# Performance work log

Hardware: AMD Instinct MI355X
Metric: run time of the kernel (lower is better)

## Reference

```python
import jax, jax.numpy as jnp
import numpy as np

B, L, C = 32, 4096, 64
PL, PC = 64, 16          # patch sizes along L and C
NP = 256                 # num_patches
OUT = 512                # output_dim
FS = 1000.0              # sampling frequency -> T = 1/FS


def setup_inputs() -> dict:
    key = jax.random.key(0)
    ks = jax.random.split(key, 7)
    d_in = PL * (PC * 2)
    return {
        "x": jax.random.normal(ks[0], (B, L, C), dtype=jnp.float32),
        "start_L": jax.random.randint(ks[1], (B, NP), 0, L - PL + 1, dtype=jnp.int32),
        "start_C": jax.random.randint(ks[2], (B, NP), 0, C - PC + 1, dtype=jnp.int32),
        "w1": jax.random.normal(ks[3], (OUT, d_in), dtype=jnp.float32) / np.sqrt(d_in),
        "b1": jax.random.normal(ks[4], (OUT,), dtype=jnp.float32) * 0.01,
        "w2": jax.random.normal(ks[5], (OUT, OUT), dtype=jnp.float32) / np.sqrt(OUT),
        "b2": jax.random.normal(ks[6], (OUT,), dtype=jnp.float32) * 0.01,
    }


def reference(x, start_L, start_C, w1, b1, w2, b2):
    T = 1.0 / FS
    t = jnp.arange(L, dtype=jnp.float32) * T                      # [L]

    # patch index grids (wrapping, as in the torch module)
    idx_L = (start_L[:, :, None] + jnp.arange(PL, dtype=jnp.int32)) % L   # [B,NP,PL]
    idx_C = (start_C[:, :, None] + jnp.arange(PC, dtype=jnp.int32)) % C   # [B,NP,PC]

    # double gather: patches[b,p,i,j] = x[b, idx_L[b,p,i], idx_C[b,p,j]]
    b_idx = jnp.arange(B, dtype=jnp.int32)[:, None, None, None]
    patches = x[b_idx, idx_L[:, :, :, None], idx_C[:, :, None, :]]        # [B,NP,PL,PC]

    # time embedding gathered with the same L indices, broadcast over PC
    t_patches = jnp.broadcast_to(t[idx_L][:, :, :, None], (B, NP, PL, PC))

    feats = jnp.concatenate([patches, t_patches], axis=-1)                # [B,NP,PL,2*PC]
    feats = feats.reshape(B, NP, PL * 2 * PC)

    h = jnp.einsum('bpd,od->bpo', feats, w1) + b1
    h = jax.nn.silu(h)
    out = jnp.einsum('bpo,qo->bpq', h, w2) + b2                           # [B,NP,OUT]
    return out
```

## Files before the change

kernel.cpp:

```cpp
#include <hip/hip_runtime.h>
#include <hip/hip_bf16.h>
#include <stdint.h>

#define LL   4096
#define CCH  64
#define DOUT 512
#define MM   8192
#define TT   0.001f

using bf16 = __hip_bfloat16;
typedef __attribute__((ext_vector_type(8))) short bf16x8;
typedef __attribute__((ext_vector_type(4))) float f32x4;

__device__ __forceinline__ uint2 pack4_bf16(float a, float b, float c, float d) {
    union { bf16 h[4]; uint2 u; } p;
    p.h[0] = __float2bfloat16(a);
    p.h[1] = __float2bfloat16(b);
    p.h[2] = __float2bfloat16(c);
    p.h[3] = __float2bfloat16(d);
    return p.u;
}

__global__ __launch_bounds__(256) void prep(
    const float* __restrict__ w1, const float* __restrict__ b1,
    const float* __restrict__ w2,
    bf16* __restrict__ w1g, bf16* __restrict__ w2g,
    float* __restrict__ A1, float* __restrict__ C1)
{
    const int blk = blockIdx.x;
    if (blk < 512) {
        int g   = blk * 256 + threadIdx.x;
        int kk0 = (g & 7) * 4;
        int col = (g >> 3) & 511;
        int ic  = g >> 12;
        int l   = ic * 2 + (kk0 >> 4);
        int j0  = kk0 & 15;
        float4 v = *(const float4*)(w1 + (size_t)col * 2048 + l * 32 + j0);
        *(uint2*)(w1g + ((size_t)(ic * 512 + col) * 32 + kk0)) =
            pack4_bf16(v.x, v.y, v.z, v.w);
    } else if (blk < 768) {
        int g   = (blk - 512) * 256 + threadIdx.x;
        int kk0 = (g & 7) * 4;
        int col = (g >> 3) & 511;
        int ic2 = g >> 12;
        float4 v = *(const float4*)(w2 + (size_t)col * 512 + ic2 * 32 + kk0);
        *(uint2*)(w2g + ((size_t)(ic2 * 512 + col) * 32 + kk0)) =
            pack4_bf16(v.x, v.y, v.z, v.w);
    } else {
        const int o = (blk - 768) * 4 + (threadIdx.x >> 6);
        const int l = threadIdx.x & 63;
        const float* wr = w1 + (size_t)o * 2048 + l * 32 + 16;
        float s0 = 0.f;
#pragma unroll
        for (int j = 0; j < 16; ++j) s0 += wr[j];
        float s1 = (float)l * s0;
#pragma unroll
        for (int off = 32; off > 0; off >>= 1) {
            s0 += __shfl_down(s0, off);
            s1 += __shfl_down(s1, off);
        }
        if (l == 0) {
            A1[o] = TT * s0;
            C1[o] = b1[o] + TT * s1;
        }
    }
}

__global__ __launch_bounds__(512, 2) void mega(
    const float* __restrict__ x, const int* __restrict__ sLg,
    const int* __restrict__ sCg, const bf16* __restrict__ w1g,
    const bf16* __restrict__ w2g, const float* __restrict__ A1,
    const float* __restrict__ C1, const float* __restrict__ b2,
    float* __restrict__ out)
{
    __shared__ __align__(16) bf16 Asm[32 * 1024];
    bf16* const Hs = Asm;

    const int t    = threadIdx.x;
    const int lane = t & 63;
    const int wave = t >> 6;
    const int fr   = lane & 15;
    const int fq   = lane >> 4;
    const int m0   = blockIdx.x * 32;
    const int b    = m0 >> 8;

    {
        const int gr  = t >> 4;
        const int gs  = t & 15;
        const int gsl = sLg[m0 + gr];
        const int gsc = sCg[m0 + gr];
        const float* gx = x + ((size_t)b * LL + gsl + (gs >> 2)) * CCH
                            + gsc + (gs & 3) * 4;
        float4 xv[16];
#pragma unroll
        for (int p = 0; p < 16; ++p)
            xv[p] = *(const float4*)(gx + (size_t)p * 4 * CCH);
#pragma unroll
        for (int p = 0; p < 16; ++p) {
            const int l = 4 * p + (gs >> 2);
            const int u = l * 2 + ((gs & 3) >> 1);
            const int idx = gr * 1024 + ((u ^ (gr & 7)) * 8) + (gs & 1) * 4;
            *(uint2*)(Asm + idx) = pack4_bf16(xv[p].x, xv[p].y, xv[p].z, xv[p].w);
        }
    }
    __syncthreads();

    const bf16* const w1base = w1g + (size_t)(wave * 64 + fr) * 32 + fq * 8;
    f32x4 acc[2][4] = {};
    {
        bf16x8 bnx[4];
#pragma unroll
        for (int j = 0; j < 4; ++j)
            bnx[j] = *(const bf16x8*)(w1base + j * 512);
#pragma unroll
        for (int it = 0; it < 32; ++it) {
            bf16x8 bcur[4];
#pragma unroll
            for (int j = 0; j < 4; ++j) bcur[j] = bnx[j];
            if (it < 31) {
                const bf16* p = w1base + (size_t)(it + 1) * 16384;
#pragma unroll
                for (int j = 0; j < 4; ++j)
                    bnx[j] = *(const bf16x8*)(p + j * 512);
            }
            bf16x8 af[2];
#pragma unroll
            for (int i = 0; i < 2; ++i) {
                const int row = i * 16 + fr;
                const int u   = it * 4 + fq;
                af[i] = *(const bf16x8*)&Asm[row * 1024 + ((u ^ (row & 7)) * 8)];
            }
#pragma unroll
            for (int i = 0; i < 2; ++i)
#pragma unroll
                for (int j = 0; j < 4; ++j)
                    acc[i][j] = __builtin_amdgcn_mfma_f32_16x16x32_bf16(
                        af[i], bcur[j], acc[i][j], 0, 0, 0);
        }
    }
    __syncthreads();

    {
        float slr[2][4];
#pragma unroll
        for (int i = 0; i < 2; ++i)
#pragma unroll
            for (int rr = 0; rr < 4; ++rr)
                slr[i][rr] = (float)sLg[m0 + i * 16 + fq * 4 + rr];
#pragma unroll
        for (int j = 0; j < 4; ++j) {
            const int col = wave * 64 + j * 16 + fr;
            const float av = A1[col];
            const float cv = C1[col];
            const int c8 = col >> 3, c7 = col & 7;
#pragma unroll
            for (int i = 0; i < 2; ++i)
#pragma unroll
                for (int rr = 0; rr < 4; ++rr) {
                    const int row = i * 16 + fq * 4 + rr;
                    float v = acc[i][j][rr] + slr[i][rr] * av + cv;
                    v = v / (1.0f + __expf(-v));
                    Hs[row * 512 + ((c8 ^ (row & 7)) * 8) + c7] = __float2bfloat16(v);
                }
        }
    }
    __syncthreads();

    const bf16* const w2base = w2g + (size_t)(wave * 64 + fr) * 32 + fq * 8;
    f32x4 acc2[2][4] = {};
    {
        bf16x8 bnx[4];
#pragma unroll
        for (int j = 0; j < 4; ++j)
            bnx[j] = *(const bf16x8*)(w2base + j * 512);
#pragma unroll
        for (int it2 = 0; it2 < 16; ++it2) {
            bf16x8 bcur[4];
#pragma unroll
            for (int j = 0; j < 4; ++j) bcur[j] = bnx[j];
            if (it2 < 15) {
                const bf16* p = w2base + (size_t)(it2 + 1) * 16384;
#pragma unroll
                for (int j = 0; j < 4; ++j)
                    bnx[j] = *(const bf16x8*)(p + j * 512);
            }
            bf16x8 af[2];
#pragma unroll
            for (int i = 0; i < 2; ++i) {
                const int row = i * 16 + fr;
                const int u2  = it2 * 4 + fq;
                af[i] = *(const bf16x8*)&Hs[row * 512 + ((u2 ^ (row & 7)) * 8)];
            }
#pragma unroll
            for (int i = 0; i < 2; ++i)
#pragma unroll
                for (int j = 0; j < 4; ++j)
                    acc2[i][j] = __builtin_amdgcn_mfma_f32_16x16x32_bf16(
                        af[i], bcur[j], acc2[i][j], 0, 0, 0);
        }
    }

#pragma unroll
    for (int j = 0; j < 4; ++j) {
        const int col = wave * 64 + j * 16 + fr;
        const float bv = b2[col];
#pragma unroll
        for (int i = 0; i < 2; ++i)
#pragma unroll
            for (int rr = 0; rr < 4; ++rr) {
                const int row = m0 + i * 16 + fq * 4 + rr;
                out[(size_t)row * 512 + col] = acc2[i][j][rr] + bv;
            }
    }
}

extern "C" void kernel_launch(void* const* d_in, const int* in_sizes, int n_in,
                              void* d_out, int out_size, void* d_ws, size_t ws_size,
                              hipStream_t stream)
{
    const float* x  = (const float*)d_in[0];
    const int*   sL = (const int*)  d_in[1];
    const int*   sC = (const int*)  d_in[2];
    const float* w1 = (const float*)d_in[3];
    const float* b1 = (const float*)d_in[4];
    const float* w2 = (const float*)d_in[5];
    const float* b2 = (const float*)d_in[6];
    float* out = (float*)d_out;

    char* ws = (char*)d_ws;
    bf16*  w1g = (bf16*)ws;
    bf16*  w2g = (bf16*)(ws + (1 << 20));
    float* A1  = (float*)(ws + (1 << 20) + (1 << 19));
    float* C1  = A1 + DOUT;

    prep<<<896, 256, 0, stream>>>(w1, b1, w2, w1g, w2g, A1, C1);
    mega<<<MM / 32, 512, 0, stream>>>(x, sL, sC, w1g, w2g, A1, C1, b2, out);
}
```

Measured before the change: 123.5 us.

## Deepen weight prefetch to four stages and double-buffer LDS A fragments

Both GEMM loops now keep four iterations of weight fragments in flight in registers instead of one, and load the next iteration's LDS A fragments before issuing the current MFMAs. The second-GEMM weight prefetch, the A1/C1/b2 loads and the start_L values (cached in LDS) are moved earlier so they overlap the first GEMM epilogue. The aim is to hide global load latency under the MFMAs. The cost is many more VGPRs (16 bf16x8 per buffer), which could cause spills or lower occupancy under launch_bounds(512,2).

```diff
diff --git a/kernel.cpp b/kernel.cpp
--- a/kernel.cpp
+++ b/kernel.cpp
@@ -74,6 +74,7 @@
     float* __restrict__ out)
 {
     __shared__ __align__(16) bf16 Asm[32 * 1024];
+    __shared__ float slf[32];
     bf16* const Hs = Asm;
 
     const int t    = threadIdx.x;
@@ -89,6 +90,7 @@
         const int gs  = t & 15;
         const int gsl = sLg[m0 + gr];
         const int gsc = sCg[m0 + gr];
+        if (gs == 0) slf[gr] = (float)gsl;
         const float* gx = x + ((size_t)b * LL + gsl + (gs >> 2)) * CCH
                             + gsc + (gs & 3) * 4;
         float4 xv[16];
@@ -108,27 +110,37 @@
     const bf16* const w1base = w1g + (size_t)(wave * 64 + fr) * 32 + fq * 8;
     f32x4 acc[2][4] = {};
     {
-        bf16x8 bnx[4];
-#pragma unroll
-        for (int j = 0; j < 4; ++j)
-            bnx[j] = *(const bf16x8*)(w1base + j * 512);
+        bf16x8 bnx[4][4];
+#pragma unroll
+        for (int d = 0; d < 4; ++d)
+#pragma unroll
+            for (int j = 0; j < 4; ++j)
+                bnx[d][j] = *(const bf16x8*)(w1base + (size_t)d * 16384 + j * 512);
+        bf16x8 af[2];
+#pragma unroll
+        for (int i = 0; i < 2; ++i) {
+            const int row = i * 16 + fr;
+            af[i] = *(const bf16x8*)&Asm[row * 1024 + ((fq ^ (row & 7)) * 8)];
+        }
 #pragma unroll
         for (int it = 0; it < 32; ++it) {
             bf16x8 bcur[4];
 #pragma unroll
-            for (int j = 0; j < 4; ++j) bcur[j] = bnx[j];
+            for (int j = 0; j < 4; ++j) bcur[j] = bnx[it & 3][j];
+            if (it < 28) {
+                const bf16* p = w1base + (size_t)(it + 4) * 16384;
+#pragma unroll
+                for (int j = 0; j < 4; ++j)
+                    bnx[it & 3][j] = *(const bf16x8*)(p + j * 512);
+            }
+            bf16x8 afn[2];
             if (it < 31) {
-                const bf16* p = w1base + (size_t)(it + 1) * 16384;
-#pragma unroll
-                for (int j = 0; j < 4; ++j)
-                    bnx[j] = *(const bf16x8*)(p + j * 512);
-            }
-            bf16x8 af[2];
-#pragma unroll
-            for (int i = 0; i < 2; ++i) {
-                const int row = i * 16 + fr;
-                const int u   = it * 4 + fq;
-                af[i] = *(const bf16x8*)&Asm[row * 1024 + ((u ^ (row & 7)) * 8)];
+#pragma unroll
+                for (int i = 0; i < 2; ++i) {
+                    const int row = i * 16 + fr;
+                    const int u   = (it + 1) * 4 + fq;
+                    afn[i] = *(const bf16x8*)&Asm[row * 1024 + ((u ^ (row & 7)) * 8)];
+                }
             }
 #pragma unroll
             for (int i = 0; i < 2; ++i)
@@ -136,22 +148,41 @@
                 for (int j = 0; j < 4; ++j)
                     acc[i][j] = __builtin_amdgcn_mfma_f32_16x16x32_bf16(
                         af[i], bcur[j], acc[i][j], 0, 0, 0);
+            if (it < 31) {
+#pragma unroll
+                for (int i = 0; i < 2; ++i) af[i] = afn[i];
+            }
         }
     }
     __syncthreads();
 
+    const bf16* const w2base = w2g + (size_t)(wave * 64 + fr) * 32 + fq * 8;
+    bf16x8 bnx2[4][4];
+#pragma unroll
+    for (int d = 0; d < 4; ++d)
+#pragma unroll
+        for (int j = 0; j < 4; ++j)
+            bnx2[d][j] = *(const bf16x8*)(w2base + (size_t)d * 16384 + j * 512);
+    float avv[4], cvv[4];
+#pragma unroll
+    for (int j = 0; j < 4; ++j) {
+        const int col = wave * 64 + j * 16 + fr;
+        avv[j] = A1[col];
+        cvv[j] = C1[col];
+    }
+
     {
         float slr[2][4];
 #pragma unroll
         for (int i = 0; i < 2; ++i)
 #pragma unroll
             for (int rr = 0; rr < 4; ++rr)
-                slr[i][rr] = (float)sLg[m0 + i * 16 + fq * 4 + rr];
+                slr[i][rr] = slf[i * 16 + fq * 4 + rr];
 #pragma unroll
         for (int j = 0; j < 4; ++j) {
             const int col = wave * 64 + j * 16 + fr;
-            const float av = A1[col];
-            const float cv = C1[col];
+            const float av = avv[j];
+            const float cv = cvv[j];
             const int c8 = col >> 3, c7 = col & 7;
 #pragma unroll
             for (int i = 0; i < 2; ++i)
@@ -166,44 +197,54 @@
     }
     __syncthreads();
 
-    const bf16* const w2base = w2g + (size_t)(wave * 64 + fr) * 32 + fq * 8;
     f32x4 acc2[2][4] = {};
-    {
-        bf16x8 bnx[4];
-#pragma unroll
-        for (int j = 0; j < 4; ++j)
-            bnx[j] = *(const bf16x8*)(w2base + j * 512);
+    float bvv[4];
+#pragma unroll
+    for (int j = 0; j < 4; ++j) bvv[j] = b2[wave * 64 + j * 16 + fr];
+    {
+        bf16x8 af2[2];
+#pragma unroll
+        for (int i = 0; i < 2; ++i) {
+            const int row = i * 16 + fr;
+            af2[i] = *(const bf16x8*)&Hs[row * 512 + ((fq ^ (row & 7)) * 8)];
+        }
 #pragma unroll
         for (int it2 = 0; it2 < 16; ++it2) {
             bf16x8 bcur[4];
 #pragma unroll
-            for (int j = 0; j < 4; ++j) bcur[j] = bnx[j];
+            for (int j = 0; j < 4; ++j) bcur[j] = bnx2[it2 & 3][j];
+            if (it2 < 12) {
+                const bf16* p = w2base + (size_t)(it2 + 4) * 16384;
+#pragma unroll
+                for (int j = 0; j < 4; ++j)
+                    bnx2[it2 & 3][j] = *(const bf16x8*)(p + j * 512);
+            }
+            bf16x8 afn[2];
             if (it2 < 15) {
-                const bf16* p = w2base + (size_t)(it2 + 1) * 16384;
-#pragma unroll
-                for (int j = 0; j < 4; ++j)
-                    bnx[j] = *(const bf16x8*)(p + j * 512);
-            }
-            bf16x8 af[2];
-#pragma unroll
-            for (int i = 0; i < 2; ++i) {
-                const int row = i * 16 + fr;
-                const int u2  = it2 * 4 + fq;
-                af[i] = *(const bf16x8*)&Hs[row * 512 + ((u2 ^ (row & 7)) * 8)];
+#pragma unroll
+                for (int i = 0; i < 2; ++i) {
+                    const int row = i * 16 + fr;
+                    const int u2  = (it2 + 1) * 4 + fq;
+                    afn[i] = *(const bf16x8*)&Hs[row * 512 + ((u2 ^ (row & 7)) * 8)];
+                }
             }
 #pragma unroll
             for (int i = 0; i < 2; ++i)
 #pragma unroll
                 for (int j = 0; j < 4; ++j)
                     acc2[i][j] = __builtin_amdgcn_mfma_f32_16x16x32_bf16(
-                        af[i], bcur[j], acc2[i][j], 0, 0, 0);
+                        af2[i], bcur[j], acc2[i][j], 0, 0, 0);
+            if (it2 < 15) {
+#pragma unroll
+                for (int i = 0; i < 2; ++i) af2[i] = afn[i];
+            }
         }
     }
 
 #pragma unroll
     for (int j = 0; j < 4; ++j) {
         const int col = wave * 64 + j * 16 + fr;
-        const float bv = b2[col];
+        const float bv = bvv[j];
 #pragma unroll
         for (int i = 0; i < 2; ++i)
 #pragma unroll
```

New measurement: 121.4 us. No clear change (-1.6%).

## Double block threads to 1024 and halve per-wave column tile

Applied to the files above, without the earlier changes.

Launches 16 waves per block, each owning 32 output columns instead of 64, with a wider gather mapping. It also hoists the second GEMM weight prefetch and the bias/affine loads ahead of the SiLU stage, and caches start_L in shared memory. The aim is more waves to hide memory latency and overlap of weight loads with the activation stage. The tighter launch bounds may restrict registers and cause spills, and each wave reuses the A fragments less.

```diff
diff --git a/kernel.cpp b/kernel.cpp
--- a/kernel.cpp
+++ b/kernel.cpp
@@ -66,7 +66,7 @@
     }
 }
 
-__global__ __launch_bounds__(512, 2) void mega(
+__global__ __launch_bounds__(1024, 4) void mega(
     const float* __restrict__ x, const int* __restrict__ sLg,
     const int* __restrict__ sCg, const bf16* __restrict__ w1g,
     const bf16* __restrict__ w2g, const float* __restrict__ A1,
@@ -74,6 +74,7 @@
     float* __restrict__ out)
 {
     __shared__ __align__(16) bf16 Asm[32 * 1024];
+    __shared__ float slf[32];
     bf16* const Hs = Asm;
 
     const int t    = threadIdx.x;
@@ -85,42 +86,45 @@
     const int b    = m0 >> 8;
 
     {
-        const int gr  = t >> 4;
-        const int gs  = t & 15;
+        const int gr  = t >> 5;
+        const int gs  = t & 31;
         const int gsl = sLg[m0 + gr];
         const int gsc = sCg[m0 + gr];
-        const float* gx = x + ((size_t)b * LL + gsl + (gs >> 2)) * CCH
-                            + gsc + (gs & 3) * 4;
-        float4 xv[16];
-#pragma unroll
-        for (int p = 0; p < 16; ++p)
-            xv[p] = *(const float4*)(gx + (size_t)p * 4 * CCH);
-#pragma unroll
-        for (int p = 0; p < 16; ++p) {
-            const int l = 4 * p + (gs >> 2);
-            const int u = l * 2 + ((gs & 3) >> 1);
-            const int idx = gr * 1024 + ((u ^ (gr & 7)) * 8) + (gs & 1) * 4;
+        if (gs == 0) slf[gr] = (float)gsl;
+        const int c4 = gs & 3;
+        const int l0 = gs >> 2;
+        const float* gx = x + ((size_t)b * LL + gsl + l0) * CCH
+                            + gsc + c4 * 4;
+        float4 xv[8];
+#pragma unroll
+        for (int p = 0; p < 8; ++p)
+            xv[p] = *(const float4*)(gx + (size_t)p * 8 * CCH);
+#pragma unroll
+        for (int p = 0; p < 8; ++p) {
+            const int l = p * 8 + l0;
+            const int u = l * 2 + (c4 >> 1);
+            const int idx = gr * 1024 + ((u ^ (gr & 7)) * 8) + (c4 & 1) * 4;
             *(uint2*)(Asm + idx) = pack4_bf16(xv[p].x, xv[p].y, xv[p].z, xv[p].w);
         }
     }
     __syncthreads();
 
-    const bf16* const w1base = w1g + (size_t)(wave * 64 + fr) * 32 + fq * 8;
-    f32x4 acc[2][4] = {};
-    {
-        bf16x8 bnx[4];
-#pragma unroll
-        for (int j = 0; j < 4; ++j)
+    const bf16* const w1base = w1g + (size_t)(wave * 32 + fr) * 32 + fq * 8;
+    f32x4 acc[2][2] = {};
+    {
+        bf16x8 bnx[2];
+#pragma unroll
+        for (int j = 0; j < 2; ++j)
             bnx[j] = *(const bf16x8*)(w1base + j * 512);
 #pragma unroll
         for (int it = 0; it < 32; ++it) {
-            bf16x8 bcur[4];
-#pragma unroll
-            for (int j = 0; j < 4; ++j) bcur[j] = bnx[j];
+            bf16x8 bcur[2];
+#pragma unroll
+            for (int j = 0; j < 2; ++j) bcur[j] = bnx[j];
             if (it < 31) {
                 const bf16* p = w1base + (size_t)(it + 1) * 16384;
 #pragma unroll
-                for (int j = 0; j < 4; ++j)
+                for (int j = 0; j < 2; ++j)
                     bnx[j] = *(const bf16x8*)(p + j * 512);
             }
             bf16x8 af[2];
@@ -133,25 +137,38 @@
 #pragma unroll
             for (int i = 0; i < 2; ++i)
 #pragma unroll
-                for (int j = 0; j < 4; ++j)
+                for (int j = 0; j < 2; ++j)
                     acc[i][j] = __builtin_amdgcn_mfma_f32_16x16x32_bf16(
                         af[i], bcur[j], acc[i][j], 0, 0, 0);
         }
     }
     __syncthreads();
 
+    const bf16* const w2base = w2g + (size_t)(wave * 32 + fr) * 32 + fq * 8;
+    bf16x8 bnx2[2];
+#pragma unroll
+    for (int j = 0; j < 2; ++j)
+        bnx2[j] = *(const bf16x8*)(w2base + j * 512);
+    float avv[2], cvv[2];
+#pragma unroll
+    for (int j = 0; j < 2; ++j) {
+        const int col = wave * 32 + j * 16 + fr;
+        avv[j] = A1[col];
+        cvv[j] = C1[col];
+    }
+
     {
         float slr[2][4];
 #pragma unroll
         for (int i = 0; i < 2; ++i)
 #pragma unroll
             for (int rr = 0; rr < 4; ++rr)
-                slr[i][rr] = (float)sLg[m0 + i * 16 + fq * 4 + rr];
-#pragma unroll
-        for (int j = 0; j < 4; ++j) {
-            const int col = wave * 64 + j * 16 + fr;
-            const float av = A1[col];
-            const float cv = C1[col];
+                slr[i][rr] = slf[i * 16 + fq * 4 + rr];
+#pragma unroll
+        for (int j = 0; j < 2; ++j) {
+            const int col = wave * 32 + j * 16 + fr;
+            const float av = avv[j];
+            const float cv = cvv[j];
             const int c8 = col >> 3, c7 = col & 7;
 #pragma unroll
             for (int i = 0; i < 2; ++i)
@@ -166,44 +183,42 @@
     }
     __syncthreads();
 
-    const bf16* const w2base = w2g + (size_t)(wave * 64 + fr) * 32 + fq * 8;
-    f32x4 acc2[2][4] = {};
-    {
-        bf16x8 bnx[4];
-#pragma unroll
-        for (int j = 0; j < 4; ++j)
-            bnx[j] = *(const bf16x8*)(w2base + j * 512);
+    f32x4 acc2[2][2] = {};
+    float bvv[2];
+#pragma unroll
+    for (int j = 0; j < 2; ++j) bvv[j] = b2[wave * 32 + j * 16 + fr];
+    {
 #pragma unroll
         for (int it2 = 0; it2 < 16; ++it2) {
-            bf16x8 bcur[4];
-#pragma unroll
-            for (int j = 0; j < 4; ++j) bcur[j] = bnx[j];
+            bf16x8 bcur[2];
+#pragma unroll
+            for (int j = 0; j < 2; ++j) bcur[j] = bnx2[j];
             if (it2 < 15) {
                 const bf16* p = w2base + (size_t)(it2 + 1) * 16384;
 #pragma unroll
-                for (int j = 0; j < 4; ++j)
-                    bnx[j] = *(const bf16x8*)(p + j * 512);
-            }
-            bf16x8 af[2];
+                for (int j = 0; j < 2; ++j)
+                    bnx2[j] = *(const bf16x8*)(p + j * 512);
+            }
+            bf16x8 af2[2];
 #pragma unroll
             for (int i = 0; i < 2; ++i) {
                 const int row = i * 16 + fr;
                 const int u2  = it2 * 4 + fq;
-                af[i] = *(const bf16x8*)&Hs[row * 512 + ((u2 ^ (row & 7)) * 8)];
+                af2[i] = *(const bf16x8*)&Hs[row * 512 + ((u2 ^ (row & 7)) * 8)];
             }
 #pragma unroll
             for (int i = 0; i < 2; ++i)
 #pragma unroll
-                for (int j = 0; j < 4; ++j)
+                for (int j = 0; j < 2; ++j)
                     acc2[i][j] = __builtin_amdgcn_mfma_f32_16x16x32_bf16(
-                        af[i], bcur[j], acc2[i][j], 0, 0, 0);
-        }
-    }
-
-#pragma unroll
-    for (int j = 0; j < 4; ++j) {
-        const int col = wave * 64 + j * 16 + fr;
-        const float bv = b2[col];
+                        af2[i], bcur[j], acc2[i][j], 0, 0, 0);
+        }
+    }
+
+#pragma unroll
+    for (int j = 0; j < 2; ++j) {
+        const int col = wave * 32 + j * 16 + fr;
+        const float bv = bvv[j];
 #pragma unroll
         for (int i = 0; i < 2; ++i)
 #pragma unroll
@@ -234,5 +249,5 @@
     float* C1  = A1 + DOUT;
 
     prep<<<896, 256, 0, stream>>>(w1, b1, w2, w1g, w2g, A1, C1);
-    mega<<<MM / 32, 512, 0, stream>>>(x, sL, sC, w1g, w2g, A1, C1, b2, out);
-}
+    mega<<<MM / 32, 1024, 0, stream>>>(x, sL, sC, w1g, w2g, A1, C1, b2, out);
+}
```

Measured after the change: 123.9 us. Within noise of the previous version (+0.3%).

## Deepen weight prefetch to 4-stage register ring with manual vmcnt waits

Applied to the files above, without the earlier changes.

Replaces the one-deep weight prefetch with a four-stage register ring of global loads issued through inline asm, gated by explicit s_waitcnt vmcnt counts. W1 prefetch now starts before the x gather, and W2 prefetch is issued before the SiLU epilogue. K-chunk start is rotated per wave and block to spread L2 accesses. Bias and A1/C1 loads are hoisted, and sLg is staged in LDS. This raises register pressure, and the hand-counted vmcnt values must match the compiler's other outstanding loads to stay correct.

```diff
diff --git a/kernel.cpp b/kernel.cpp
--- a/kernel.cpp
+++ b/kernel.cpp
@@ -19,6 +19,12 @@
     p.h[2] = __float2bfloat16(c);
     p.h[3] = __float2bfloat16(d);
     return p.u;
+}
+
+__device__ __forceinline__ bf16x8 gload16(const bf16* p) {
+    bf16x8 r;
+    asm volatile("global_load_dwordx4 %0, %1, off" : "=v"(r) : "v"(p));
+    return r;
 }
 
 __global__ __launch_bounds__(256) void prep(
@@ -74,6 +80,7 @@
     float* __restrict__ out)
 {
     __shared__ __align__(16) bf16 Asm[32 * 1024];
+    __shared__ float slf[32];
     bf16* const Hs = Asm;
 
     const int t    = threadIdx.x;
@@ -84,11 +91,29 @@
     const int m0   = blockIdx.x * 32;
     const int b    = m0 >> 8;
 
+    const int coff = blockIdx.x >> 3;
+    const int ca0  = (wave * 4 + coff) & 31;
+    const int cb0  = (wave * 2 + coff) & 15;
+
+    const bf16* const w1base = w1g + (size_t)(wave * 64 + fr) * 32 + fq * 8;
+    const bf16* const w2base = w2g + (size_t)(wave * 64 + fr) * 32 + fq * 8;
+
+    bf16x8 ring[4][4];
+#pragma unroll
+    for (int k = 0; k < 4; ++k) {
+        const int c = (ca0 + k) & 31;
+        const bf16* p = w1base + (size_t)c * 16384;
+#pragma unroll
+        for (int j = 0; j < 4; ++j)
+            ring[k][j] = gload16(p + j * 512);
+    }
+
     {
         const int gr  = t >> 4;
         const int gs  = t & 15;
         const int gsl = sLg[m0 + gr];
         const int gsc = sCg[m0 + gr];
+        if (gs == 0) slf[gr] = (float)gsl;
         const float* gx = x + ((size_t)b * LL + gsl + (gs >> 2)) * CCH
                             + gsc + (gs & 3) * 4;
         float4 xv[16];
@@ -103,42 +128,62 @@
             *(uint2*)(Asm + idx) = pack4_bf16(xv[p].x, xv[p].y, xv[p].z, xv[p].w);
         }
     }
+
+    float avv[4], cvv[4], bvv[4];
+#pragma unroll
+    for (int j = 0; j < 4; ++j) {
+        const int col = wave * 64 + j * 16 + fr;
+        avv[j] = A1[col];
+        cvv[j] = C1[col];
+        bvv[j] = b2[col];
+    }
     __syncthreads();
 
-    const bf16* const w1base = w1g + (size_t)(wave * 64 + fr) * 32 + fq * 8;
     f32x4 acc[2][4] = {};
-    {
-        bf16x8 bnx[4];
+#pragma unroll
+    for (int it = 0; it < 32; ++it) {
+        if (it <= 28)      { asm volatile("s_waitcnt vmcnt(12)"); }
+        else if (it == 29) { asm volatile("s_waitcnt vmcnt(8)"); }
+        else if (it == 30) { asm volatile("s_waitcnt vmcnt(4)"); }
+        else               { asm volatile("s_waitcnt vmcnt(0)"); }
+        __builtin_amdgcn_sched_barrier(0);
+        const int c = (ca0 + it) & 31;
+        bf16x8 bcur[4];
+#pragma unroll
+        for (int j = 0; j < 4; ++j) bcur[j] = ring[it & 3][j];
+        if (it < 28) {
+            const int cn = (ca0 + it + 4) & 31;
+            const bf16* p = w1base + (size_t)cn * 16384;
+#pragma unroll
+            for (int j = 0; j < 4; ++j)
+                ring[it & 3][j] = gload16(p + j * 512);
+        }
+        bf16x8 af[2];
+#pragma unroll
+        for (int i = 0; i < 2; ++i) {
+            const int row = i * 16 + fr;
+            const int u   = c * 4 + fq;
+            af[i] = *(const bf16x8*)&Asm[row * 1024 + ((u ^ (row & 7)) * 8)];
+        }
+#pragma unroll
+        for (int i = 0; i < 2; ++i)
+#pragma unroll
+            for (int j = 0; j < 4; ++j)
+                acc[i][j] = __builtin_amdgcn_mfma_f32_16x16x32_bf16(
+                    af[i], bcur[j], acc[i][j], 0, 0, 0);
+    }
+
+#pragma unroll
+    for (int k = 0; k < 4; ++k) {
+        const int c = (cb0 + k) & 15;
+        const bf16* p = w2base + (size_t)c * 16384;
 #pragma unroll
         for (int j = 0; j < 4; ++j)
-            bnx[j] = *(const bf16x8*)(w1base + j * 512);
-#pragma unroll
-        for (int it = 0; it < 32; ++it) {
-            bf16x8 bcur[4];
-#pragma unroll
-            for (int j = 0; j < 4; ++j) bcur[j] = bnx[j];
-            if (it < 31) {
-                const bf16* p = w1base + (size_t)(it + 1) * 16384;
-#pragma unroll
-                for (int j = 0; j < 4; ++j)
-                    bnx[j] = *(const bf16x8*)(p + j * 512);
-            }
-            bf16x8 af[2];
-#pragma unroll
-            for (int i = 0; i < 2; ++i) {
-                const int row = i * 16 + fr;
-                const int u   = it * 4 + fq;
-                af[i] = *(const bf16x8*)&Asm[row * 1024 + ((u ^ (row & 7)) * 8)];
-            }
-#pragma unroll
-            for (int i = 0; i < 2; ++i)
-#pragma unroll
-                for (int j = 0; j < 4; ++j)
-                    acc[i][j] = __builtin_amdgcn_mfma_f32_16x16x32_bf16(
-                        af[i], bcur[j], acc[i][j], 0, 0, 0);
-        }
-    }
-    __syncthreads();
+            ring[k][j] = gload16(p + j * 512);
+    }
+    asm volatile("s_waitcnt lgkmcnt(0)" ::: "memory");
+    __builtin_amdgcn_s_barrier();
+    __builtin_amdgcn_sched_barrier(0);
 
     {
         float slr[2][4];
@@ -146,12 +191,12 @@
         for (int i = 0; i < 2; ++i)
 #pragma unroll
             for (int rr = 0; rr < 4; ++rr)
-                slr[i][rr] = (float)sLg[m0 + i * 16 + fq * 4 + rr];
+                slr[i][rr] = slf[i * 16 + fq * 4 + rr];
 #pragma unroll
         for (int j = 0; j < 4; ++j) {
             const int col = wave * 64 + j * 16 + fr;
-            const float av = A1[col];
-            const float cv = C1[col];
+            const float av = avv[j];
+            const float cv = cvv[j];
             const int c8 = col >> 3, c7 = col & 7;
 #pragma unroll
             for (int i = 0; i < 2; ++i)
@@ -164,46 +209,48 @@
                 }
         }
     }
-    __syncthreads();
-
-    const bf16* const w2base = w2g + (size_t)(wave * 64 + fr) * 32 + fq * 8;
+    asm volatile("s_waitcnt lgkmcnt(0)" ::: "memory");
+    __builtin_amdgcn_s_barrier();
+    __builtin_amdgcn_sched_barrier(0);
+
     f32x4 acc2[2][4] = {};
-    {
-        bf16x8 bnx[4];
-#pragma unroll
-        for (int j = 0; j < 4; ++j)
-            bnx[j] = *(const bf16x8*)(w2base + j * 512);
-#pragma unroll
-        for (int it2 = 0; it2 < 16; ++it2) {
-            bf16x8 bcur[4];
-#pragma unroll
-            for (int j = 0; j < 4; ++j) bcur[j] = bnx[j];
-            if (it2 < 15) {
-                const bf16* p = w2base + (size_t)(it2 + 1) * 16384;
-#pragma unroll
-                for (int j = 0; j < 4; ++j)
-                    bnx[j] = *(const bf16x8*)(p + j * 512);
-            }
-            bf16x8 af[2];
-#pragma unroll
-            for (int i = 0; i < 2; ++i) {
-                const int row = i * 16 + fr;
-                const int u2  = it2 * 4 + fq;
-                af[i] = *(const bf16x8*)&Hs[row * 512 + ((u2 ^ (row & 7)) * 8)];
-            }
-#pragma unroll
-            for (int i = 0; i < 2; ++i)
-#pragma unroll
-                for (int j = 0; j < 4; ++j)
-                    acc2[i][j] = __builtin_amdgcn_mfma_f32_16x16x32_bf16(
-                        af[i], bcur[j], acc2[i][j], 0, 0, 0);
-        }
+#pragma unroll
+    for (int it2 = 0; it2 < 16; ++it2) {
+        if (it2 <= 12)      { asm volatile("s_waitcnt vmcnt(12)"); }
+        else if (it2 == 13) { asm volatile("s_waitcnt vmcnt(8)"); }
+        else if (it2 == 14) { asm volatile("s_waitcnt vmcnt(4)"); }
+        else                { asm volatile("s_waitcnt vmcnt(0)"); }
+        __builtin_amdgcn_sched_barrier(0);
+        const int c = (cb0 + it2) & 15;
+        bf16x8 bcur[4];
+#pragma unroll
+        for (int j = 0; j < 4; ++j) bcur[j] = ring[it2 & 3][j];
+        if (it2 < 12) {
+            const int cn = (cb0 + it2 + 4) & 15;
+            const bf16* p = w2base + (size_t)cn * 16384;
+#pragma unroll
+            for (int j = 0; j < 4; ++j)
+                ring[it2 & 3][j] = gload16(p + j * 512);
+        }
+        bf16x8 af2[2];
+#pragma unroll
+        for (int i = 0; i < 2; ++i) {
+            const int row = i * 16 + fr;
+            const int u2  = c * 4 + fq;
+            af2[i] = *(const bf16x8*)&Hs[row * 512 + ((u2 ^ (row & 7)) * 8)];
+        }
+#pragma unroll
+        for (int i = 0; i < 2; ++i)
+#pragma unroll
+            for (int j = 0; j < 4; ++j)
+                acc2[i][j] = __builtin_amdgcn_mfma_f32_16x16x32_bf16(
+                    af2[i], bcur[j], acc2[i][j], 0, 0, 0);
     }
 
 #pragma unroll
     for (int j = 0; j < 4; ++j) {
         const int col = wave * 64 + j * 16 + fr;
-        const float bv = b2[col];
+        const float bv = bvv[j];
 #pragma unroll
         for (int i = 0; i < 2; ++i)
 #pragma unroll
```

After: 123.9 us. Within noise of the previous version (+0.3%).
